# Kernel optimization log

Measured on AMD Instinct MI355X. Metric: run time of the kernel, lower is better.

Reference implementation:

```python
import jax, jax.numpy as jnp
import numpy as np

THRESH = -np.log(0.7).astype(np.float32)  # module stores -log(thresh)
MIN_KEPT = 100000
IGNORE_INDEX = 255


def setup_inputs() -> dict:
    key = jax.random.key(0)
    k1, k2 = jax.random.split(key)
    N, C, H, W = 8, 19, 512, 1024
    logits = jax.random.normal(k1, (N, C, H, W), dtype=jnp.float32)
    labels = jax.random.randint(k2, (N, H, W), 0, C, dtype=jnp.int32)
    return {"logits": logits, "labels": labels}


def reference(logits, labels):
    # per-pixel cross entropy, reduction='none', ignore_index -> 0 loss
    logp = jax.nn.log_softmax(logits, axis=1)                 # [N,C,H,W]
    lbl = jnp.clip(labels, 0, logits.shape[1] - 1)
    nll = -jnp.take_along_axis(logp, lbl[:, None], axis=1)[:, 0]  # [N,H,W]
    valid = labels != IGNORE_INDEX
    loss = jnp.where(valid, nll, 0.0).reshape(-1)             # [N*H*W]

    # sort descending (torch.sort descending=True)
    sorted_desc = jnp.sort(loss)[::-1]

    cond = sorted_desc[MIN_KEPT] > THRESH

    # branch 1: mean over all losses > thresh
    mask = (sorted_desc > THRESH).astype(sorted_desc.dtype)
    mean_thresh = jnp.sum(sorted_desc * mask) / jnp.sum(mask)

    # branch 2: mean over top min_kept losses
    mean_topk = jnp.mean(sorted_desc[:MIN_KEPT])

    return jnp.where(cond, mean_thresh, mean_topk)
```

## Files before the change

kernel.cpp:

```cpp
#include <hip/hip_runtime.h>

#define THRESH     0.35667494393873245f
#define K_KEPT     100000
#define IGNORE_IDX 255
#define C_         19
#define HW_        524288
#define LOG_HW     19
#define M_         4194304

#define OFF_HIST   8388608
#define OFF_SCAL   8519680
#define ZERO_BYTES (131072 + 64)

#define HOT_LO 15360u
#define HOT_N  2048u

#define GRID_MAIN 1024
#define GRID_SUM  512

__global__ __launch_bounds__(256) void ohem_main(
    const float* __restrict__ logits, const int* __restrict__ labels,
    unsigned short* __restrict__ lossb, unsigned int* __restrict__ hist,
    double* __restrict__ sum_gt, unsigned long long* __restrict__ cnt_gt)
{
    __shared__ unsigned int lh[HOT_N];
    for (unsigned int i = threadIdx.x; i < HOT_N; i += 256) lh[i] = 0;
    __syncthreads();

    double lsum = 0.0;
    unsigned int lcnt = 0;

    const int stride = GRID_MAIN * 256;
    for (int g = blockIdx.x * 256 + threadIdx.x; g < (M_ / 4); g += stride) {
        const int p0   = g << 2;
        const int n    = p0 >> LOG_HW;
        const int rest = p0 & (HW_ - 1);
        const float* base = logits + (size_t)n * ((size_t)C_ * HW_) + rest;

        const int4 lb4 = *reinterpret_cast<const int4*>(labels + p0);
        const int lb[4] = {lb4.x, lb4.y, lb4.z, lb4.w};
        int cl[4];
        #pragma unroll
        for (int j = 0; j < 4; ++j) cl[j] = min(max(lb[j], 0), C_ - 1);

        float s[4]  = {0.f, 0.f, 0.f, 0.f};
        float xl[4] = {0.f, 0.f, 0.f, 0.f};
        #pragma unroll
        for (int c = 0; c < C_; ++c) {
            const float4 v = *reinterpret_cast<const float4*>(base + (size_t)c * HW_);
            s[0] += __expf(v.x);  xl[0] = (cl[0] == c) ? v.x : xl[0];
            s[1] += __expf(v.y);  xl[1] = (cl[1] == c) ? v.y : xl[1];
            s[2] += __expf(v.z);  xl[2] = (cl[2] == c) ? v.z : xl[2];
            s[3] += __expf(v.w);  xl[3] = (cl[3] == c) ? v.w : xl[3];
        }

        unsigned short ob[4];
        #pragma unroll
        for (int j = 0; j < 4; ++j) {
            const float nll = __logf(s[j]) - xl[j];
            const float L = (lb[j] != IGNORE_IDX) ? fmaxf(nll, 0.f) : 0.f;
            if (L > THRESH) { lsum += (double)L; ++lcnt; }
            const unsigned int b = __float_as_uint(L);
            const unsigned int bin = (b + 0x7FFFu + ((b >> 16) & 1u)) >> 16;
            ob[j] = (unsigned short)bin;
            if (bin - HOT_LO < HOT_N) atomicAdd(&lh[bin - HOT_LO], 1u);
            else                      atomicAdd(&hist[bin], 1u);
        }
        ushort4 ov; ov.x = ob[0]; ov.y = ob[1]; ov.z = ob[2]; ov.w = ob[3];
        *reinterpret_cast<ushort4*>(lossb + p0) = ov;
    }

    __syncthreads();
    for (unsigned int i = threadIdx.x; i < HOT_N; i += 256) {
        const unsigned int v = lh[i];
        if (v) atomicAdd(&hist[HOT_LO + i], v);
    }

    for (int off = 32; off > 0; off >>= 1) {
        lsum += __shfl_down(lsum, off);
        lcnt += __shfl_down(lcnt, off);
    }
    __shared__ double       wsum[4];
    __shared__ unsigned int wcnt[4];
    const int wid = threadIdx.x >> 6, lane = threadIdx.x & 63;
    if (lane == 0) { wsum[wid] = lsum; wcnt[wid] = lcnt; }
    __syncthreads();
    if (threadIdx.x == 0) {
        atomicAdd(sum_gt, wsum[0] + wsum[1] + wsum[2] + wsum[3]);
        atomicAdd(cnt_gt, (unsigned long long)wcnt[0] + wcnt[1] + wcnt[2] + wcnt[3]);
    }
}

__global__ __launch_bounds__(256) void ohem_select(
    const unsigned int* __restrict__ hist, unsigned int* __restrict__ sel)
{
    __shared__ unsigned int part[256];
    __shared__ unsigned int sfx[257];
    __shared__ int schunk;
    __shared__ unsigned int scum;

    const int t = threadIdx.x;
    const unsigned int target = K_KEPT + 1u;

    unsigned int s = 0;
    const unsigned int* hp = hist + t * 128;
    #pragma unroll 8
    for (int i = 0; i < 128; ++i) s += hp[i];
    part[t] = s;
    sfx[t] = s;
    if (t == 0) sfx[256] = 0;
    __syncthreads();
    for (int off = 1; off < 256; off <<= 1) {
        const unsigned int v = (t + off < 256) ? sfx[t + off] : 0;
        __syncthreads();
        sfx[t] += v;
        __syncthreads();
    }
    if (sfx[t] >= target && (t == 255 || sfx[t + 1] < target)) {
        schunk = t;
        scum = sfx[t] - part[t];
    }
    __syncthreads();
    const int ch = schunk;
    const unsigned int above_chunk = scum;
    __syncthreads();
    if (t < 128) sfx[t] = hist[ch * 128 + t];
    if (t == 0) sfx[128] = 0;
    __syncthreads();
    for (int off = 1; off < 128; off <<= 1) {
        unsigned int v = 0;
        if (t < 128) v = (t + off < 128) ? sfx[t + off] : 0;
        __syncthreads();
        if (t < 128) sfx[t] += v;
        __syncthreads();
    }
    if (t < 128) {
        const unsigned int incl  = above_chunk + sfx[t];
        const unsigned int above = above_chunk + ((t < 127) ? sfx[t + 1] : 0);
        if (incl >= target && above < target) {
            sel[2] = (unsigned int)(ch * 128 + t);
            sel[3] = above;
        }
    }
}

__global__ __launch_bounds__(256) void ohem_sumgt(
    const unsigned int* __restrict__ lossu, const unsigned int* __restrict__ sel,
    double* __restrict__ sum_gt_vk)
{
    const unsigned int vkb = sel[2];
    double lsum = 0.0;
    const int stride = GRID_SUM * 256;
    const uint4* lp = reinterpret_cast<const uint4*>(lossu);
    for (int g = blockIdx.x * 256 + threadIdx.x; g < (M_ / 8); g += stride) {
        const uint4 u = lp[g];
        float acc = 0.f;
        #pragma unroll
        for (int w = 0; w < 4; ++w) {
            const unsigned int uw = (&u.x)[w];
            const unsigned int lo = uw & 0xFFFFu, hi = uw >> 16;
            if (lo > vkb) acc += __uint_as_float(lo << 16);
            if (hi > vkb) acc += __uint_as_float(hi << 16);
        }
        lsum += (double)acc;
    }
    for (int off = 32; off > 0; off >>= 1) lsum += __shfl_down(lsum, off);
    __shared__ double wsum[4];
    const int wid = threadIdx.x >> 6, lane = threadIdx.x & 63;
    if (lane == 0) wsum[wid] = lsum;
    __syncthreads();
    if (threadIdx.x == 0)
        atomicAdd(sum_gt_vk, wsum[0] + wsum[1] + wsum[2] + wsum[3]);
}

__global__ void ohem_finalize(const unsigned int* __restrict__ sel,
                              const double* __restrict__ sum_gt,
                              const unsigned long long* __restrict__ cnt_gt,
                              const double* __restrict__ sum_gt_vk,
                              float* __restrict__ out)
{
    if (threadIdx.x == 0) {
        const float vk = __uint_as_float(sel[2] << 16);
        double r;
        if (vk > THRESH) {
            r = sum_gt[0] / (double)cnt_gt[0];
        } else {
            const unsigned int c = sel[3];
            r = (sum_gt_vk[0] + (double)(K_KEPT - (long long)c) * (double)vk)
                / (double)K_KEPT;
        }
        out[0] = (float)r;
    }
}

extern "C" void kernel_launch(void* const* d_in, const int* in_sizes, int n_in,
                              void* d_out, int out_size, void* d_ws, size_t ws_size,
                              hipStream_t stream)
{
    const float* logits = (const float*)d_in[0];
    const int*   labels = (const int*)d_in[1];
    float* out = (float*)d_out;

    char* ws = (char*)d_ws;
    unsigned short*     lossb     = (unsigned short*)ws;
    unsigned int*       hist      = (unsigned int*)(ws + OFF_HIST);
    char*               scal      = ws + OFF_SCAL;
    double*             sum_gt    = (double*)(scal + 0);
    double*             sum_gt_vk = (double*)(scal + 8);
    unsigned long long* cnt_gt    = (unsigned long long*)(scal + 16);
    unsigned int*       sel       = (unsigned int*)(scal + 24);

    hipMemsetAsync(hist, 0, ZERO_BYTES, stream);

    ohem_main    <<<GRID_MAIN, 256, 0, stream>>>(logits, labels, lossb, hist,
                                                 sum_gt, cnt_gt);
    ohem_select  <<<1, 256, 0, stream>>>(hist, sel);
    ohem_sumgt   <<<GRID_SUM, 256, 0, stream>>>((const unsigned int*)lossb, sel,
                                                sum_gt_vk);
    ohem_finalize<<<1, 64, 0, stream>>>(sel, sum_gt, cnt_gt, sum_gt_vk, out);
}
```

Baseline: 93.20 us.

## Compute top-k sum from histogram and drop the per-pixel loss buffer pass

The sum of losses above the k-th value is now taken from the bf16-rounded histogram (count times bin value) inside the select kernel, not by re-reading a stored per-pixel loss buffer. This removes the 8 MB loss write in the main kernel, the separate sumgt and finalize launches, and their reads. The exp accumulation is also split into two interleaved accumulators to shorten the dependency chain. The result is still bf16-quantised as before, and the single select block now scans the histogram twice.

```diff
diff --git a/kernel.cpp b/kernel.cpp
--- a/kernel.cpp
+++ b/kernel.cpp
@@ -8,19 +8,17 @@
 #define LOG_HW     19
 #define M_         4194304
 
-#define OFF_HIST   8388608
-#define OFF_SCAL   8519680
+#define OFF_SCAL   131072
 #define ZERO_BYTES (131072 + 64)
 
 #define HOT_LO 15360u
 #define HOT_N  2048u
 
 #define GRID_MAIN 1024
-#define GRID_SUM  512
 
 __global__ __launch_bounds__(256) void ohem_main(
     const float* __restrict__ logits, const int* __restrict__ labels,
-    unsigned short* __restrict__ lossb, unsigned int* __restrict__ hist,
+    unsigned int* __restrict__ hist,
     double* __restrict__ sum_gt, unsigned long long* __restrict__ cnt_gt)
 {
     __shared__ unsigned int lh[HOT_N];
@@ -43,31 +41,35 @@
         #pragma unroll
         for (int j = 0; j < 4; ++j) cl[j] = min(max(lb[j], 0), C_ - 1);
 
-        float s[4]  = {0.f, 0.f, 0.f, 0.f};
+        float sa[4] = {0.f, 0.f, 0.f, 0.f};
+        float sb[4] = {0.f, 0.f, 0.f, 0.f};
         float xl[4] = {0.f, 0.f, 0.f, 0.f};
         #pragma unroll
         for (int c = 0; c < C_; ++c) {
             const float4 v = *reinterpret_cast<const float4*>(base + (size_t)c * HW_);
-            s[0] += __expf(v.x);  xl[0] = (cl[0] == c) ? v.x : xl[0];
-            s[1] += __expf(v.y);  xl[1] = (cl[1] == c) ? v.y : xl[1];
-            s[2] += __expf(v.z);  xl[2] = (cl[2] == c) ? v.z : xl[2];
-            s[3] += __expf(v.w);  xl[3] = (cl[3] == c) ? v.w : xl[3];
+            if (c & 1) {
+                sb[0] += __expf(v.x); sb[1] += __expf(v.y);
+                sb[2] += __expf(v.z); sb[3] += __expf(v.w);
+            } else {
+                sa[0] += __expf(v.x); sa[1] += __expf(v.y);
+                sa[2] += __expf(v.z); sa[3] += __expf(v.w);
+            }
+            xl[0] = (cl[0] == c) ? v.x : xl[0];
+            xl[1] = (cl[1] == c) ? v.y : xl[1];
+            xl[2] = (cl[2] == c) ? v.z : xl[2];
+            xl[3] = (cl[3] == c) ? v.w : xl[3];
         }
 
-        unsigned short ob[4];
         #pragma unroll
         for (int j = 0; j < 4; ++j) {
-            const float nll = __logf(s[j]) - xl[j];
+            const float nll = __logf(sa[j] + sb[j]) - xl[j];
             const float L = (lb[j] != IGNORE_IDX) ? fmaxf(nll, 0.f) : 0.f;
             if (L > THRESH) { lsum += (double)L; ++lcnt; }
             const unsigned int b = __float_as_uint(L);
             const unsigned int bin = (b + 0x7FFFu + ((b >> 16) & 1u)) >> 16;
-            ob[j] = (unsigned short)bin;
             if (bin - HOT_LO < HOT_N) atomicAdd(&lh[bin - HOT_LO], 1u);
             else                      atomicAdd(&hist[bin], 1u);
         }
-        ushort4 ov; ov.x = ob[0]; ov.y = ob[1]; ov.z = ob[2]; ov.w = ob[3];
-        *reinterpret_cast<ushort4*>(lossb + p0) = ov;
     }
 
     __syncthreads();
@@ -91,13 +93,18 @@
     }
 }
 
-__global__ __launch_bounds__(256) void ohem_select(
-    const unsigned int* __restrict__ hist, unsigned int* __restrict__ sel)
+__global__ __launch_bounds__(256) void ohem_select_final(
+    const unsigned int* __restrict__ hist,
+    const double* __restrict__ sum_gt,
+    const unsigned long long* __restrict__ cnt_gt,
+    float* __restrict__ out)
 {
     __shared__ unsigned int part[256];
     __shared__ unsigned int sfx[257];
     __shared__ int schunk;
     __shared__ unsigned int scum;
+    __shared__ unsigned int svkb, sabove;
+    __shared__ double wred[4];
 
     const int t = threadIdx.x;
     const unsigned int target = K_KEPT + 1u;
@@ -125,7 +132,6 @@
     const unsigned int above_chunk = scum;
     __syncthreads();
     if (t < 128) sfx[t] = hist[ch * 128 + t];
-    if (t == 0) sfx[128] = 0;
     __syncthreads();
     for (int off = 1; off < 128; off <<= 1) {
         unsigned int v = 0;
@@ -138,55 +144,32 @@
         const unsigned int incl  = above_chunk + sfx[t];
         const unsigned int above = above_chunk + ((t < 127) ? sfx[t + 1] : 0);
         if (incl >= target && above < target) {
-            sel[2] = (unsigned int)(ch * 128 + t);
-            sel[3] = above;
+            svkb   = (unsigned int)(ch * 128 + t);
+            sabove = above;
         }
     }
-}
+    __syncthreads();
+    const unsigned int vkb = svkb, above = sabove;
 
-__global__ __launch_bounds__(256) void ohem_sumgt(
-    const unsigned int* __restrict__ lossu, const unsigned int* __restrict__ sel,
-    double* __restrict__ sum_gt_vk)
-{
-    const unsigned int vkb = sel[2];
-    double lsum = 0.0;
-    const int stride = GRID_SUM * 256;
-    const uint4* lp = reinterpret_cast<const uint4*>(lossu);
-    for (int g = blockIdx.x * 256 + threadIdx.x; g < (M_ / 8); g += stride) {
-        const uint4 u = lp[g];
-        float acc = 0.f;
-        #pragma unroll
-        for (int w = 0; w < 4; ++w) {
-            const unsigned int uw = (&u.x)[w];
-            const unsigned int lo = uw & 0xFFFFu, hi = uw >> 16;
-            if (lo > vkb) acc += __uint_as_float(lo << 16);
-            if (hi > vkb) acc += __uint_as_float(hi << 16);
-        }
-        lsum += (double)acc;
+    double w = 0.0;
+    for (int i = 0; i < 128; ++i) {
+        const unsigned int bin = (unsigned int)(t * 128 + i);
+        const unsigned int c = hp[i];
+        if (bin > vkb && c)
+            w += (double)c * (double)__uint_as_float(bin << 16);
     }
-    for (int off = 32; off > 0; off >>= 1) lsum += __shfl_down(lsum, off);
-    __shared__ double wsum[4];
-    const int wid = threadIdx.x >> 6, lane = threadIdx.x & 63;
-    if (lane == 0) wsum[wid] = lsum;
+    for (int off = 32; off > 0; off >>= 1) w += __shfl_down(w, off);
+    const int wid = t >> 6, lane = t & 63;
+    if (lane == 0) wred[wid] = w;
     __syncthreads();
-    if (threadIdx.x == 0)
-        atomicAdd(sum_gt_vk, wsum[0] + wsum[1] + wsum[2] + wsum[3]);
-}
-
-__global__ void ohem_finalize(const unsigned int* __restrict__ sel,
-                              const double* __restrict__ sum_gt,
-                              const unsigned long long* __restrict__ cnt_gt,
-                              const double* __restrict__ sum_gt_vk,
-                              float* __restrict__ out)
-{
-    if (threadIdx.x == 0) {
-        const float vk = __uint_as_float(sel[2] << 16);
+    if (t == 0) {
+        const double wsumv = wred[0] + wred[1] + wred[2] + wred[3];
+        const float vk = __uint_as_float(vkb << 16);
         double r;
         if (vk > THRESH) {
             r = sum_gt[0] / (double)cnt_gt[0];
         } else {
-            const unsigned int c = sel[3];
-            r = (sum_gt_vk[0] + (double)(K_KEPT - (long long)c) * (double)vk)
+            r = (wsumv + (double)(K_KEPT - (long long)above) * (double)vk)
                 / (double)K_KEPT;
         }
         out[0] = (float)r;
@@ -202,20 +185,14 @@
     float* out = (float*)d_out;
 
     char* ws = (char*)d_ws;
-    unsigned short*     lossb     = (unsigned short*)ws;
-    unsigned int*       hist      = (unsigned int*)(ws + OFF_HIST);
-    char*               scal      = ws + OFF_SCAL;
-    double*             sum_gt    = (double*)(scal + 0);
-    double*             sum_gt_vk = (double*)(scal + 8);
-    unsigned long long* cnt_gt    = (unsigned long long*)(scal + 16);
-    unsigned int*       sel       = (unsigned int*)(scal + 24);
+    unsigned int*       hist   = (unsigned int*)ws;
+    char*               scal   = ws + OFF_SCAL;
+    double*             sum_gt = (double*)(scal + 0);
+    unsigned long long* cnt_gt = (unsigned long long*)(scal + 8);
 
     hipMemsetAsync(hist, 0, ZERO_BYTES, stream);
 
-    ohem_main    <<<GRID_MAIN, 256, 0, stream>>>(logits, labels, lossb, hist,
-                                                 sum_gt, cnt_gt);
-    ohem_select  <<<1, 256, 0, stream>>>(hist, sel);
-    ohem_sumgt   <<<GRID_SUM, 256, 0, stream>>>((const unsigned int*)lossb, sel,
-                                                sum_gt_vk);
-    ohem_finalize<<<1, 64, 0, stream>>>(sel, sum_gt, cnt_gt, sum_gt_vk, out);
+    ohem_main        <<<GRID_MAIN, 256, 0, stream>>>(logits, labels, hist,
+                                                     sum_gt, cnt_gt);
+    ohem_select_final<<<1, 256, 0, stream>>>(hist, sum_gt, cnt_gt, out);
 }
```

Measured after the change: 86.86 us. -6.8%, faster.
